# Performance work log

Hardware: AMD Instinct MI355X
Metric: run time of the kernel (lower is better)

The kernel has to match this reference:

```python
import jax, jax.numpy as jnp
import numpy as np

HEADS = 6
G = 4  # redundant group repeat factor in the original module
EPS = 1e-5


def _dw_bn(x, w, gamma, beta, mean, var):
    # depthwise 3x3 conv (stride 1, pad 1, no bias) + BatchNorm (eval mode)
    C = x.shape[1]
    y = jax.lax.conv_general_dilated(
        x, w, window_strides=(1, 1), padding=[(1, 1), (1, 1)],
        dimension_numbers=('NCHW', 'OIHW', 'NCHW'), feature_group_count=C)
    inv = gamma / jnp.sqrt(var + EPS)
    return y * inv[None, :, None, None] + (beta - mean * inv)[None, :, None, None]


def setup_inputs() -> dict:
    key = jax.random.key(0)
    ks = jax.random.split(key, 20)
    B, Cin, Cout, H, W = 8, 192, 192, 28, 28
    inp = {
        'x': jax.random.normal(ks[0], (B, H * W, Cin), jnp.float32),
        'h': H, 'w': W,
    }
    s = 0.1
    for i, p in enumerate(['q', 'k', 'v']):
        inp[f'dw{p}_w'] = jax.random.normal(ks[1 + i], (Cin, 1, 3, 3), jnp.float32) * s
        bk = jax.random.split(ks[4 + i], 4)
        inp[f'bn{p}_g'] = 1.0 + 0.1 * jax.random.normal(bk[0], (Cin,), jnp.float32)
        inp[f'bn{p}_b'] = 0.1 * jax.random.normal(bk[1], (Cin,), jnp.float32)
        inp[f'bn{p}_m'] = 0.1 * jax.random.normal(bk[2], (Cin,), jnp.float32)
        inp[f'bn{p}_v'] = jax.random.uniform(bk[3], (Cin,), jnp.float32, 0.5, 1.5)
        inp[f'p{p}_w'] = jax.random.normal(ks[7 + i], (Cout, Cin), jnp.float32) * (Cin ** -0.5)
        inp[f'p{p}_b'] = 0.01 * jax.random.normal(ks[10 + i], (Cout,), jnp.float32)
    inp['po_w'] = jax.random.normal(ks[13], (Cout, Cout), jnp.float32) * (Cout ** -0.5)
    inp['po_b'] = 0.01 * jax.random.normal(ks[14], (Cout,), jnp.float32)
    return inp


def reference(x, h, w,
              dwq_w, bnq_g, bnq_b, bnq_m, bnq_v, pq_w, pq_b,
              dwk_w, bnk_g, bnk_b, bnk_m, bnk_v, pk_w, pk_b,
              dwv_w, bnv_g, bnv_b, bnv_m, bnv_v, pv_w, pv_b,
              po_w, po_b):
    B, N, Cin = x.shape
    Cout = pq_w.shape[0]
    ch = Cout // HEADS  # per-head channel dim
    x4 = jnp.transpose(x, (0, 2, 1)).reshape(B, Cin, h, w)

    q = _dw_bn(x4, dwq_w, bnq_g, bnq_b, bnq_m, bnq_v)
    k = _dw_bn(x4, dwk_w, bnk_g, bnk_b, bnk_m, bnk_v)
    v = _dw_bn(x4, dwv_w, bnv_g, bnv_b, bnv_m, bnv_v)

    # 1x1 conv projections
    q = jnp.einsum('oc,bcij->boij', pq_w, q) + pq_b[None, :, None, None]
    k = jnp.einsum('oc,bcij->boij', pk_w, k) + pk_b[None, :, None, None]
    v = jnp.einsum('oc,bcij->boij', pv_w, v) + pv_b[None, :, None, None]

    # split heads: channels are (head, ch) ordered -> (B, heads, ch, h, w)
    qh = q.reshape(B, HEADS, ch, h, w)
    kh = k.reshape(B, HEADS, ch, h, w)
    vh = v.reshape(B, HEADS, ch, h, w)

    scale = Cout ** -0.5  # NOTE: original scales by dim_out**-0.5, not head_dim
    score = jnp.einsum('bhcij,bhckl->bhijkl', qh, kh) * scale
    attn = jax.nn.softmax(score.reshape(B, HEADS, h, w, h * w), axis=-1)
    attn = attn.reshape(B, HEADS, h, w, h, w)

    out = jnp.einsum('bhijkl,bhckl->bhcij', attn, vh)  # (B, heads, ch, h, w)
    # original output channel order is (ch, heads) via 'b c h g i j -> b (c h) g i j'
    out = jnp.transpose(out, (0, 2, 1, 3, 4))  # (B, ch, heads, h, w)
    out = jnp.broadcast_to(out[:, :, :, None], (B, ch, HEADS, G, h, w))
    out = out.reshape(B, ch * HEADS, G, h, w)

    y = jnp.einsum('oc,bcgij->bogij', po_w, out) + po_b[None, :, None, None, None]
    return y
```

## Files before the change

kernel.cpp:

```cpp
#include <hip/hip_runtime.h>
#include <math.h>

namespace {
constexpr int kB = 8;
constexpr int kC = 192;
constexpr int kH = 28;
constexpr int kW = 28;
constexpr int kN = 784;
constexpr int kHEADS = 6;
constexpr int kG = 4;
constexpr float kEPS = 1e-5f;
constexpr float kQS = 0.07216878364870322f * 1.4426950408889634f;
constexpr int kNP = 800;
}

typedef __attribute__((ext_vector_type(8))) short bf16x8;
typedef __attribute__((ext_vector_type(4))) float f32x4;

union VU { ushort4 hlf[2]; bf16x8 v; };

static __device__ __forceinline__ unsigned short f2bf(float f) {
    union { float f; unsigned int u; } v; v.f = f;
    unsigned int r = v.u + 0x7fffu + ((v.u >> 16) & 1u);
    return (unsigned short)(r >> 16);
}

static __device__ __forceinline__ float fexp2(float x) {
    return __builtin_amdgcn_exp2f(x);
}

__global__ __launch_bounds__(256) void prep_kernel(
    const float* __restrict__ pqw, const float* __restrict__ pkw,
    const float* __restrict__ pvw, const float* __restrict__ pow_,
    unsigned short* __restrict__ Wq, unsigned short* __restrict__ Wk,
    unsigned short* __restrict__ Wv, unsigned short* __restrict__ Wo)
{
    const int aux = blockIdx.x * 256 + threadIdx.x;
    const int e0 = aux * 4;
    const int mat = e0 / (kC * kC);
    const int r = e0 % (kC * kC);
    if (mat < 3) {
        const float* src = (mat == 0) ? pqw : (mat == 1) ? pkw : pvw;
        unsigned short* dst = (mat == 0) ? Wq : (mat == 1) ? Wk : Wv;
        const f32x4 v = *(const f32x4*)&src[r];
        ushort4 p;
        p.x = f2bf(v[0]); p.y = f2bf(v[1]); p.z = f2bf(v[2]); p.w = f2bf(v[3]);
        *(ushort4*)&dst[r] = p;
    } else {
        const int o = r / kC, c0 = r % kC;
        ushort4 p;
        unsigned short* pp = &p.x;
#pragma unroll
        for (int e = 0; e < 4; ++e) {
            const int c = c0 + e;
            pp[e] = f2bf(pow_[o * kC + (c & 31) * kHEADS + (c >> 5)]);
        }
        *(ushort4*)&Wo[o * kC + c0] = p;
    }
}

__global__ __launch_bounds__(768, 6) void dwproj_kernel(
    const float* __restrict__ x,
    const float* __restrict__ wq, const float* __restrict__ gq,
    const float* __restrict__ bq, const float* __restrict__ mq,
    const float* __restrict__ vq,
    const float* __restrict__ wk, const float* __restrict__ gk,
    const float* __restrict__ bk, const float* __restrict__ mk,
    const float* __restrict__ vk,
    const float* __restrict__ wv, const float* __restrict__ gv,
    const float* __restrict__ bv, const float* __restrict__ mv,
    const float* __restrict__ vv,
    const unsigned short* __restrict__ Wq, const unsigned short* __restrict__ Wk,
    const unsigned short* __restrict__ Wv,
    const float* __restrict__ pqb, const float* __restrict__ pkb,
    const float* __restrict__ pvb,
    unsigned short* __restrict__ Qb, unsigned short* __restrict__ Kb,
    unsigned short* __restrict__ Vb)
{
    __shared__ unsigned short Xs[3][16][200];

    const int b  = blockIdx.x / 49;
    const int n0 = (blockIdx.x % 49) * 16;
    const int t = threadIdx.x;

    {
        const int c  = t % 192;
        const int ph = t / 192;
        float wwq[9], wwk[9], wwv[9];
#pragma unroll
        for (int i = 0; i < 9; ++i) {
            wwq[i] = wq[c * 9 + i];
            wwk[i] = wk[c * 9 + i];
            wwv[i] = wv[c * 9 + i];
        }
        const float invq = gq[c] * rsqrtf(vq[c] + kEPS);
        const float addq = bq[c] - mq[c] * invq;
        const float invk = gk[c] * rsqrtf(vk[c] + kEPS);
        const float addk = bk[c] - mk[c] * invk;
        const float invv = gv[c] * rsqrtf(vv[c] + kEPS);
        const float addv = bv[c] - mv[c] * invv;
        const float* xb = x + (size_t)b * kN * kC + c;
#pragma unroll
        for (int p = 0; p < 4; ++p) {
            const int pos = ph * 4 + p;
            const int n = n0 + pos;
            const int i = n / kW, j = n % kW;
            float aq = 0.f, ak = 0.f, av = 0.f;
#pragma unroll
            for (int di = -1; di <= 1; ++di) {
                const int ii = i + di;
                if (ii < 0 || ii >= kH) continue;
#pragma unroll
                for (int dj = -1; dj <= 1; ++dj) {
                    const int jj = j + dj;
                    if (jj < 0 || jj >= kW) continue;
                    const float xvl = xb[(size_t)(ii * kW + jj) * kC];
                    const int tap = (di + 1) * 3 + (dj + 1);
                    aq += xvl * wwq[tap];
                    ak += xvl * wwk[tap];
                    av += xvl * wwv[tap];
                }
            }
            Xs[0][pos][c] = f2bf(aq * invq + addq);
            Xs[1][pos][c] = f2bf(ak * invk + addk);
            Xs[2][pos][c] = f2bf(av * invv + addv);
        }
    }
    __syncthreads();

    const int w = t >> 6, l = t & 63, q16 = l & 15, u = l >> 4;
#pragma unroll
    for (int k3 = 0; k3 < 3; ++k3) {
        const int unit = w * 3 + k3;
        const int br = unit / 12;
        const int ob = (unit % 12) * 16;
        const unsigned short* W = (br == 0) ? Wq : (br == 1) ? Wk : Wv;
        const float* bias       = (br == 0) ? pqb : (br == 1) ? pkb : pvb;

        f32x4 acc = {0.f, 0.f, 0.f, 0.f};
        const unsigned short* Wr = W + (size_t)(ob + q16) * kC + u * 8;
#pragma unroll
        for (int kk = 0; kk < 6; ++kk) {
            const bf16x8 wa = *(const bf16x8*)(Wr + kk * 32);
            const bf16x8 xa = *(const bf16x8*)&Xs[br][q16][u * 8 + kk * 32];
            acc = __builtin_amdgcn_mfma_f32_16x16x32_bf16(wa, xa, acc, 0, 0, 0);
        }
        const int hh = ob >> 5;
        const int ch0 = (ob & 31) + 4 * u;
        const f32x4 bi = *(const f32x4*)&bias[ob + 4 * u];
        const int n = n0 + q16;
        if (br < 2) {
            const float sc = (br == 0) ? kQS : 1.0f;
            ushort4 p;
            p.x = f2bf((acc[0] + bi[0]) * sc);
            p.y = f2bf((acc[1] + bi[1]) * sc);
            p.z = f2bf((acc[2] + bi[2]) * sc);
            p.w = f2bf((acc[3] + bi[3]) * sc);
            unsigned short* dst = ((br == 0) ? Qb : Kb) +
                ((size_t)(b * kHEADS + hh) * kNP + n) * 32 + ch0;
            *(ushort4*)dst = p;
        } else {
            unsigned short* dst = Vb +
                ((size_t)(b * kHEADS + hh) * 32 + ch0) * kNP + n;
            dst[0 * kNP] = f2bf(acc[0] + bi[0]);
            dst[1 * kNP] = f2bf(acc[1] + bi[1]);
            dst[2 * kNP] = f2bf(acc[2] + bi[2]);
            dst[3 * kNP] = f2bf(acc[3] + bi[3]);
        }
    }
}

__global__ __launch_bounds__(768, 6) void attnout_kernel(
    const unsigned short* __restrict__ Qbf, const unsigned short* __restrict__ Kbf,
    const unsigned short* __restrict__ Vbf, const unsigned short* __restrict__ Wo,
    const float* __restrict__ pob, float* __restrict__ Y)
{
    __shared__ unsigned short AOs[16][200];
    __shared__ float Mrg[6][64][9];

    const int b  = blockIdx.x / 49;
    const int i0 = (blockIdx.x % 49) * 16;
    const int t = threadIdx.x;
    const int w = t >> 6;
    const int h = w % 6;
    const int s = w / 6;
    const int l = t & 63;
    const int q16 = l & 15;
    const int u = l >> 4;

    const unsigned short* Qp = Qbf + ((size_t)(b * kHEADS + h) * kNP + i0) * 32;
    const unsigned short* Kp = Kbf + (size_t)(b * kHEADS + h) * kNP * 32;
    const unsigned short* Vr0 = Vbf + ((size_t)(b * kHEADS + h) * 32 + q16) * kNP;
    const unsigned short* Vr1 = Vr0 + (size_t)16 * kNP;

    const bf16x8 qa = *(const bf16x8*)(Qp + q16 * 32 + u * 8);

    f32x4 oa0 = {0.f, 0.f, 0.f, 0.f};
    f32x4 oa1 = {0.f, 0.f, 0.f, 0.f};
    f32x4 la  = {0.f, 0.f, 0.f, 0.f};
    f32x4 lb  = {0.f, 0.f, 0.f, 0.f};

    const int tile_begin = s ? 12 : 0;
    const int tile_end   = s ? 24 : 12;

    bf16x8 kc0 = *(const bf16x8*)(Kp + (size_t)(tile_begin * 32 + q16) * 32 + u * 8);
    bf16x8 kc1 = *(const bf16x8*)(Kp + (size_t)(tile_begin * 32 + 16 + q16) * 32 + u * 8);
    bf16x8 kn0, kn1;

    for (int tile = tile_begin; tile < tile_end; ++tile) {
        const int t0 = tile * 32;
        if (tile + 1 < tile_end) {
            const int t1 = t0 + 32;
            kn0 = *(const bf16x8*)(Kp + (size_t)(t1 + q16) * 32 + u * 8);
            kn1 = *(const bf16x8*)(Kp + (size_t)(t1 + 16 + q16) * 32 + u * 8);
        }
        VU v0, v1;
        v0.hlf[0] = *(const ushort4*)(Vr0 + t0 + 4 * u);
        v0.hlf[1] = *(const ushort4*)(Vr0 + t0 + 16 + 4 * u);
        v1.hlf[0] = *(const ushort4*)(Vr1 + t0 + 4 * u);
        v1.hlf[1] = *(const ushort4*)(Vr1 + t0 + 16 + 4 * u);
        __builtin_amdgcn_s_setprio(1);
        f32x4 d0 = {0.f, 0.f, 0.f, 0.f};
        f32x4 d1 = {0.f, 0.f, 0.f, 0.f};
        d0 = __builtin_amdgcn_mfma_f32_16x16x32_bf16(kc0, qa, d0, 0, 0, 0);
        d1 = __builtin_amdgcn_mfma_f32_16x16x32_bf16(kc1, qa, d1, 0, 0, 0);
        f32x4 ve0, ve1;
        ve0[0] = fexp2(d0[0]); ve0[1] = fexp2(d0[1]);
        ve0[2] = fexp2(d0[2]); ve0[3] = fexp2(d0[3]);
        ve1[0] = fexp2(d1[0]); ve1[1] = fexp2(d1[1]);
        ve1[2] = fexp2(d1[2]); ve1[3] = fexp2(d1[3]);
        la += ve0; lb += ve1;
        union { unsigned int wd[4]; bf16x8 v; } pa;
        asm("v_cvt_pk_bf16_f32 %0, %1, %2" : "=v"(pa.wd[0]) : "v"(ve0[0]), "v"(ve0[1]));
        asm("v_cvt_pk_bf16_f32 %0, %1, %2" : "=v"(pa.wd[1]) : "v"(ve0[2]), "v"(ve0[3]));
        asm("v_cvt_pk_bf16_f32 %0, %1, %2" : "=v"(pa.wd[2]) : "v"(ve1[0]), "v"(ve1[1]));
        asm("v_cvt_pk_bf16_f32 %0, %1, %2" : "=v"(pa.wd[3]) : "v"(ve1[2]), "v"(ve1[3]));
        oa0 = __builtin_amdgcn_mfma_f32_16x16x32_bf16(pa.v, v0.v, oa0, 0, 0, 0);
        oa1 = __builtin_amdgcn_mfma_f32_16x16x32_bf16(pa.v, v1.v, oa1, 0, 0, 0);
        __builtin_amdgcn_s_setprio(0);
        kc0 = kn0; kc1 = kn1;
    }
    if (s) {
        const int t0 = 768;
        const bf16x8 ka0 = *(const bf16x8*)(Kp + (size_t)(t0 + q16) * 32 + u * 8);
        VU v0, v1;
        const ushort4 z4 = {0, 0, 0, 0};
        v0.hlf[0] = *(const ushort4*)(Vr0 + t0 + 4 * u);
        v0.hlf[1] = z4;
        v1.hlf[0] = *(const ushort4*)(Vr1 + t0 + 4 * u);
        v1.hlf[1] = z4;
        f32x4 d0 = {0.f, 0.f, 0.f, 0.f};
        d0 = __builtin_amdgcn_mfma_f32_16x16x32_bf16(ka0, qa, d0, 0, 0, 0);
        f32x4 ve0;
        ve0[0] = fexp2(d0[0]); ve0[1] = fexp2(d0[1]);
        ve0[2] = fexp2(d0[2]); ve0[3] = fexp2(d0[3]);
        la += ve0;
        union { unsigned int wd[4]; bf16x8 v; } pa;
        asm("v_cvt_pk_bf16_f32 %0, %1, %2" : "=v"(pa.wd[0]) : "v"(ve0[0]), "v"(ve0[1]));
        asm("v_cvt_pk_bf16_f32 %0, %1, %2" : "=v"(pa.wd[1]) : "v"(ve0[2]), "v"(ve0[3]));
        pa.wd[2] = 0u;
        pa.wd[3] = 0u;
        oa0 = __builtin_amdgcn_mfma_f32_16x16x32_bf16(pa.v, v0.v, oa0, 0, 0, 0);
        oa1 = __builtin_amdgcn_mfma_f32_16x16x32_bf16(pa.v, v1.v, oa1, 0, 0, 0);
    }
    float psum = ((la[0] + la[1]) + (la[2] + la[3])) +
                 ((lb[0] + lb[1]) + (lb[2] + lb[3]));

    if (s == 1) {
        float* Mp = Mrg[h][l];
        Mp[0] = oa0[0]; Mp[1] = oa0[1]; Mp[2] = oa0[2]; Mp[3] = oa0[3];
        Mp[4] = oa1[0]; Mp[5] = oa1[1]; Mp[6] = oa1[2]; Mp[7] = oa1[3];
        Mp[8] = psum;
    }
    __syncthreads();
    if (s == 0) {
        const float* Mp = Mrg[h][l];
        oa0[0] += Mp[0]; oa0[1] += Mp[1]; oa0[2] += Mp[2]; oa0[3] += Mp[3];
        oa1[0] += Mp[4]; oa1[1] += Mp[5]; oa1[2] += Mp[6]; oa1[3] += Mp[7];
        float lsum = psum + Mp[8];
        lsum += __shfl_xor(lsum, 16);
        lsum += __shfl_xor(lsum, 32);
        const float rinv = 1.0f / lsum;
        const float r0 = __shfl(rinv, u * 4 + 0);
        const float r1 = __shfl(rinv, u * 4 + 1);
        const float r2 = __shfl(rinv, u * 4 + 2);
        const float r3 = __shfl(rinv, u * 4 + 3);
        AOs[4 * u + 0][h * 32 + q16] = f2bf(oa0[0] * r0);
        AOs[4 * u + 1][h * 32 + q16] = f2bf(oa0[1] * r1);
        AOs[4 * u + 2][h * 32 + q16] = f2bf(oa0[2] * r2);
        AOs[4 * u + 3][h * 32 + q16] = f2bf(oa0[3] * r3);
        AOs[4 * u + 0][h * 32 + 16 + q16] = f2bf(oa1[0] * r0);
        AOs[4 * u + 1][h * 32 + 16 + q16] = f2bf(oa1[1] * r1);
        AOs[4 * u + 2][h * 32 + 16 + q16] = f2bf(oa1[2] * r2);
        AOs[4 * u + 3][h * 32 + 16 + q16] = f2bf(oa1[3] * r3);
    }
    __syncthreads();

    {
        const int ob = w * 16;
        f32x4 acc = {0.f, 0.f, 0.f, 0.f};
        const unsigned short* Wr = Wo + (size_t)(ob + q16) * kC + u * 8;
#pragma unroll
        for (int kk = 0; kk < 6; ++kk) {
            const bf16x8 wa = *(const bf16x8*)(Wr + kk * 32);
            const bf16x8 xa = *(const bf16x8*)&AOs[q16][u * 8 + kk * 32];
            acc = __builtin_amdgcn_mfma_f32_16x16x32_bf16(wa, xa, acc, 0, 0, 0);
        }
        const f32x4 bi = *(const f32x4*)&pob[ob + 4 * u];
        const int n = i0 + q16;
#pragma unroll
        for (int r = 0; r < 4; ++r) {
            const int o = ob + 4 * u + r;
            const float val = acc[r] + bi[r];
            float* yp = Y + (((size_t)b * kC + o) * kG) * kN + n;
            yp[0 * kN] = val;
            yp[1 * kN] = val;
            yp[2 * kN] = val;
            yp[3 * kN] = val;
        }
    }
}

extern "C" void kernel_launch(void* const* d_in, const int* in_sizes, int n_in,
                              void* d_out, int out_size, void* d_ws, size_t ws_size,
                              hipStream_t stream) {
    const float* x     = (const float*)d_in[0];
    const float* dwq_w = (const float*)d_in[3];
    const float* bnq_g = (const float*)d_in[4];
    const float* bnq_b = (const float*)d_in[5];
    const float* bnq_m = (const float*)d_in[6];
    const float* bnq_v = (const float*)d_in[7];
    const float* pq_w  = (const float*)d_in[8];
    const float* pq_b  = (const float*)d_in[9];
    const float* dwk_w = (const float*)d_in[10];
    const float* bnk_g = (const float*)d_in[11];
    const float* bnk_b = (const float*)d_in[12];
    const float* bnk_m = (const float*)d_in[13];
    const float* bnk_v = (const float*)d_in[14];
    const float* pk_w  = (const float*)d_in[15];
    const float* pk_b  = (const float*)d_in[16];
    const float* dwv_w = (const float*)d_in[17];
    const float* bnv_g = (const float*)d_in[18];
    const float* bnv_b = (const float*)d_in[19];
    const float* bnv_m = (const float*)d_in[20];
    const float* bnv_v = (const float*)d_in[21];
    const float* pv_w  = (const float*)d_in[22];
    const float* pv_b  = (const float*)d_in[23];
    const float* po_w  = (const float*)d_in[24];
    const float* po_b  = (const float*)d_in[25];

    unsigned short* ws = (unsigned short*)d_ws;
    const size_t QSZ = (size_t)kB * kHEADS * kNP * 32;
    unsigned short* Qb = ws;
    unsigned short* Kb = Qb + QSZ;
    unsigned short* Vb = Kb + QSZ;
    unsigned short* Wq = Vb + QSZ;
    unsigned short* Wk = Wq + kC * kC;
    unsigned short* Wv = Wk + kC * kC;
    unsigned short* Wo = Wv + kC * kC;

    prep_kernel<<<dim3(144), dim3(256), 0, stream>>>(
        pq_w, pk_w, pv_w, po_w, Wq, Wk, Wv, Wo);

    dwproj_kernel<<<dim3(kB * 49), dim3(768), 0, stream>>>(
        x,
        dwq_w, bnq_g, bnq_b, bnq_m, bnq_v,
        dwk_w, bnk_g, bnk_b, bnk_m, bnk_v,
        dwv_w, bnv_g, bnv_b, bnv_m, bnv_v,
        Wq, Wk, Wv, pq_b, pk_b, pv_b, Qb, Kb, Vb);

    attnout_kernel<<<dim3(kB * 49), dim3(768), 0, stream>>>(
        Qb, Kb, Vb, Wo, po_b, (float*)d_out);
}
```

Measured before the change: 71.32 us.

## Retile dwproj kernel: one Q/K/V branch per block, 64 positions per tile

The depthwise-conv and projection kernel now gives each block a single branch (Q, K or V) over 64 spatial positions instead of all three branches over 16 positions. The grid becomes 13x3x8 blocks. Each wave computes one 16-row output slice and reuses each weight fragment across four MFMA tiles, which cuts redundant projection-weight loads per position. In exchange the input x is read three times (once per branch), there are fewer blocks (312 vs 392), and the last tile carries padded positions that compute clamped duplicates.

```diff
diff --git a/kernel.cpp b/kernel.cpp
--- a/kernel.cpp
+++ b/kernel.cpp
@@ -77,35 +77,34 @@
     unsigned short* __restrict__ Qb, unsigned short* __restrict__ Kb,
     unsigned short* __restrict__ Vb)
 {
-    __shared__ unsigned short Xs[3][16][200];
-
-    const int b  = blockIdx.x / 49;
-    const int n0 = (blockIdx.x % 49) * 16;
+    __shared__ unsigned short Xs[64][200];
+
+    const int n0 = blockIdx.x * 64;
+    const int br = blockIdx.y;
+    const int b  = blockIdx.z;
     const int t = threadIdx.x;
 
     {
         const int c  = t % 192;
-        const int ph = t / 192;
-        float wwq[9], wwk[9], wwv[9];
-#pragma unroll
-        for (int i = 0; i < 9; ++i) {
-            wwq[i] = wq[c * 9 + i];
-            wwk[i] = wk[c * 9 + i];
-            wwv[i] = wv[c * 9 + i];
-        }
-        const float invq = gq[c] * rsqrtf(vq[c] + kEPS);
-        const float addq = bq[c] - mq[c] * invq;
-        const float invk = gk[c] * rsqrtf(vk[c] + kEPS);
-        const float addk = bk[c] - mk[c] * invk;
-        const float invv = gv[c] * rsqrtf(vv[c] + kEPS);
-        const float addv = bv[c] - mv[c] * invv;
+        const int pg = t / 192;
+        const float* dw = (br == 0) ? wq : (br == 1) ? wk : wv;
+        const float* g_ = (br == 0) ? gq : (br == 1) ? gk : gv;
+        const float* b_ = (br == 0) ? bq : (br == 1) ? bk : bv;
+        const float* m_ = (br == 0) ? mq : (br == 1) ? mk : mv;
+        const float* v_ = (br == 0) ? vq : (br == 1) ? vk : vv;
+        float ww[9];
+#pragma unroll
+        for (int i = 0; i < 9; ++i) ww[i] = dw[c * 9 + i];
+        const float inv = g_[c] * rsqrtf(v_[c] + kEPS);
+        const float add = b_[c] - m_[c] * inv;
         const float* xb = x + (size_t)b * kN * kC + c;
 #pragma unroll
-        for (int p = 0; p < 4; ++p) {
-            const int pos = ph * 4 + p;
-            const int n = n0 + pos;
+        for (int p = 0; p < 16; ++p) {
+            const int pos = pg * 16 + p;
+            int n = n0 + pos;
+            if (n > kN - 1) n = kN - 1;
             const int i = n / kW, j = n % kW;
-            float aq = 0.f, ak = 0.f, av = 0.f;
+            float a = 0.f;
 #pragma unroll
             for (int di = -1; di <= 1; ++di) {
                 const int ii = i + di;
@@ -114,58 +113,59 @@
                 for (int dj = -1; dj <= 1; ++dj) {
                     const int jj = j + dj;
                     if (jj < 0 || jj >= kW) continue;
-                    const float xvl = xb[(size_t)(ii * kW + jj) * kC];
-                    const int tap = (di + 1) * 3 + (dj + 1);
-                    aq += xvl * wwq[tap];
-                    ak += xvl * wwk[tap];
-                    av += xvl * wwv[tap];
+                    a += xb[(size_t)(ii * kW + jj) * kC] * ww[(di + 1) * 3 + dj + 1];
                 }
             }
-            Xs[0][pos][c] = f2bf(aq * invq + addq);
-            Xs[1][pos][c] = f2bf(ak * invk + addk);
-            Xs[2][pos][c] = f2bf(av * invv + addv);
+            Xs[pos][c] = f2bf(a * inv + add);
         }
     }
     __syncthreads();
 
     const int w = t >> 6, l = t & 63, q16 = l & 15, u = l >> 4;
-#pragma unroll
-    for (int k3 = 0; k3 < 3; ++k3) {
-        const int unit = w * 3 + k3;
-        const int br = unit / 12;
-        const int ob = (unit % 12) * 16;
-        const unsigned short* W = (br == 0) ? Wq : (br == 1) ? Wk : Wv;
-        const float* bias       = (br == 0) ? pqb : (br == 1) ? pkb : pvb;
-
-        f32x4 acc = {0.f, 0.f, 0.f, 0.f};
-        const unsigned short* Wr = W + (size_t)(ob + q16) * kC + u * 8;
-#pragma unroll
-        for (int kk = 0; kk < 6; ++kk) {
-            const bf16x8 wa = *(const bf16x8*)(Wr + kk * 32);
-            const bf16x8 xa = *(const bf16x8*)&Xs[br][q16][u * 8 + kk * 32];
-            acc = __builtin_amdgcn_mfma_f32_16x16x32_bf16(wa, xa, acc, 0, 0, 0);
-        }
-        const int hh = ob >> 5;
-        const int ch0 = (ob & 31) + 4 * u;
-        const f32x4 bi = *(const f32x4*)&bias[ob + 4 * u];
-        const int n = n0 + q16;
+    const int ob = w * 16;
+    const unsigned short* W = (br == 0) ? Wq : (br == 1) ? Wk : Wv;
+    const float* bias       = (br == 0) ? pqb : (br == 1) ? pkb : pvb;
+
+    f32x4 acc[4] = {{0,0,0,0}, {0,0,0,0}, {0,0,0,0}, {0,0,0,0}};
+    const unsigned short* Wr = W + (size_t)(ob + q16) * kC + u * 8;
+#pragma unroll
+    for (int kk = 0; kk < 6; ++kk) {
+        const bf16x8 wa = *(const bf16x8*)(Wr + kk * 32);
+        const bf16x8 x0 = *(const bf16x8*)&Xs[ 0 + q16][u * 8 + kk * 32];
+        const bf16x8 x1 = *(const bf16x8*)&Xs[16 + q16][u * 8 + kk * 32];
+        const bf16x8 x2 = *(const bf16x8*)&Xs[32 + q16][u * 8 + kk * 32];
+        const bf16x8 x3 = *(const bf16x8*)&Xs[48 + q16][u * 8 + kk * 32];
+        acc[0] = __builtin_amdgcn_mfma_f32_16x16x32_bf16(wa, x0, acc[0], 0, 0, 0);
+        acc[1] = __builtin_amdgcn_mfma_f32_16x16x32_bf16(wa, x1, acc[1], 0, 0, 0);
+        acc[2] = __builtin_amdgcn_mfma_f32_16x16x32_bf16(wa, x2, acc[2], 0, 0, 0);
+        acc[3] = __builtin_amdgcn_mfma_f32_16x16x32_bf16(wa, x3, acc[3], 0, 0, 0);
+    }
+
+    const int hh = ob >> 5;
+    const int ch0 = (ob & 31) + 4 * u;
+    const f32x4 bi = *(const f32x4*)&bias[ob + 4 * u];
+#pragma unroll
+    for (int nt = 0; nt < 4; ++nt) {
+        const int n = n0 + nt * 16 + q16;
+        if (n >= kN) continue;
+        const f32x4 A = acc[nt];
         if (br < 2) {
             const float sc = (br == 0) ? kQS : 1.0f;
             ushort4 p;
-            p.x = f2bf((acc[0] + bi[0]) * sc);
-            p.y = f2bf((acc[1] + bi[1]) * sc);
-            p.z = f2bf((acc[2] + bi[2]) * sc);
-            p.w = f2bf((acc[3] + bi[3]) * sc);
+            p.x = f2bf((A[0] + bi[0]) * sc);
+            p.y = f2bf((A[1] + bi[1]) * sc);
+            p.z = f2bf((A[2] + bi[2]) * sc);
+            p.w = f2bf((A[3] + bi[3]) * sc);
             unsigned short* dst = ((br == 0) ? Qb : Kb) +
                 ((size_t)(b * kHEADS + hh) * kNP + n) * 32 + ch0;
             *(ushort4*)dst = p;
         } else {
             unsigned short* dst = Vb +
                 ((size_t)(b * kHEADS + hh) * 32 + ch0) * kNP + n;
-            dst[0 * kNP] = f2bf(acc[0] + bi[0]);
-            dst[1 * kNP] = f2bf(acc[1] + bi[1]);
-            dst[2 * kNP] = f2bf(acc[2] + bi[2]);
-            dst[3 * kNP] = f2bf(acc[3] + bi[3]);
+            dst[0 * kNP] = f2bf(A[0] + bi[0]);
+            dst[1 * kNP] = f2bf(A[1] + bi[1]);
+            dst[2 * kNP] = f2bf(A[2] + bi[2]);
+            dst[3 * kNP] = f2bf(A[3] + bi[3]);
         }
     }
 }
@@ -362,7 +362,7 @@
     prep_kernel<<<dim3(144), dim3(256), 0, stream>>>(
         pq_w, pk_w, pv_w, po_w, Wq, Wk, Wv, Wo);
 
-    dwproj_kernel<<<dim3(kB * 49), dim3(768), 0, stream>>>(
+    dwproj_kernel<<<dim3(13, 3, kB), dim3(768), 0, stream>>>(
         x,
         dwq_w, bnq_g, bnq_b, bnq_m, bnq_v,
         dwk_w, bnk_g, bnk_b, bnk_m, bnk_v,
```

Result: slower. 92.95 us (+30.3%).
